# Optimization experiments

Measured on AMD Instinct MI355X. Metric: run time of the kernel, lower is better.

## Reference

```python
import jax, jax.numpy as jnp
import numpy as np

B = 8
S = 512  # seq_len


def setup_inputs() -> dict:
    key = jax.random.key(0)
    kx, kw, kb = jax.random.split(key, 3)
    x = jax.random.normal(kx, (B, S, S), dtype=jnp.float32)
    # Padded block of per-diagonal Linear weights: W[i, k, j] is weight[k, j]
    # of nn.Linear(i+1, i+1); entries with k > i or j > i are zero.
    i_d = jnp.arange(S)[:, None, None]
    k_d = jnp.arange(S)[None, :, None]
    j_d = jnp.arange(S)[None, None, :]
    wmask = ((k_d <= i_d) & (j_d <= i_d)).astype(jnp.float32)
    W = jax.random.normal(kw, (S, S, S), dtype=jnp.float32) * 0.02 * wmask
    bmask = (jnp.arange(S)[None, :] <= jnp.arange(S)[:, None]).astype(jnp.float32)
    b = jax.random.normal(kb, (S, S), dtype=jnp.float32) * 0.02 * bmask
    return {"x": x, "W": W, "b": b}


def reference(x, W, b):
    # For each anti-diagonal i (positions (r, i-r), r=0..i, with r+c=i<S):
    #   gather d = x[:, r, i-r], apply Linear_i: out = d @ W_i^T + b_i,
    #   scatter back reversed: x[:, r, i-r] = out[i-r]  =>  x[b,r,c]=out[b,r+c,c].
    S_ = x.shape[-1]
    i_idx = jnp.arange(S_)[:, None]   # diagonal index
    r_idx = jnp.arange(S_)[None, :]   # position along diagonal
    cols = (i_idx - r_idx) % S_
    valid = (r_idx <= i_idx)[None]                       # [1,S,S]
    # D[b, i, r] = x[b, r, i-r] for r<=i else 0
    D = jnp.where(valid, x[:, r_idx, cols], 0.0)         # [B,S,S]
    # Batched per-diagonal matmul: out[b,i,k] = sum_j W[i,k,j] D[b,i,j] + b[i,k]
    out = jnp.einsum('bij,ikj->bik', D, W) + b[None]     # [B,S,S]
    # Scatter back with reversal: x[b,r,c] = out[b, r+c, c] when r+c < S
    rr = jnp.arange(S_)[:, None]
    cc = jnp.arange(S_)[None, :]
    diag = rr + cc
    ok = (diag < S_)[None]
    new_x = jnp.where(ok, out[:, jnp.minimum(diag, S_ - 1), cc], x)
    return new_x
```

## Files before the change

kernel.cpp:

```cpp
#include <hip/hip_runtime.h>

#define S 512
#define NB 8
#define KT 128
#define JT 32

__global__ __launch_bounds__(256) void tail_copy_kernel(const float* __restrict__ x,
                                                        float* __restrict__ out) {
  int idx = blockIdx.x * 256 + threadIdx.x;
  int c = idx & (S - 1);
  int r = (idx >> 9) & (S - 1);
  if (r + c >= S) out[idx] = x[idx];
}

__global__ __launch_bounds__(256, 4) void diag_linear_kernel(const float* __restrict__ x,
                                                             const float* __restrict__ W,
                                                             const float* __restrict__ bias,
                                                             float* __restrict__ out) {
  __shared__ __align__(16) float WtBuf[JT * KT];
  __shared__ __align__(16) float DlBuf[S * NB];

  const int i  = (S - 1) - (int)blockIdx.x;
  const int k0 = (int)blockIdx.y * KT;
  if (k0 > i) return;

  const int tid  = threadIdx.x;
  const int wave = tid >> 6;
  const int lane = tid & 63;

  const int jend = (i + JT) & ~(JT - 1);
  const int T    = jend >> 5;

  for (int idx = tid; idx < jend * NB; idx += 256) {
    const int j = idx >> 3;
    const int b = idx & 7;
    DlBuf[idx] = (j <= i) ? x[b * (S * S) + j * S + (i - j)] : 0.0f;
  }

  const int kl_r = tid & (KT - 1);
  const int h    = tid >> 7;
  const int  k_r     = k0 + kl_r;
  const bool krow_ok = (k_r <= i);
  const float* wrow  = W + ((size_t)i * S + k_r) * S + (h << 4);

  float acc[2][NB];
#pragma unroll
  for (int m = 0; m < 2; ++m)
#pragma unroll
    for (int b = 0; b < NB; ++b) acc[m][b] = 0.0f;

  float4 v[2][4];
  if (!krow_ok) {
#pragma unroll
    for (int g = 0; g < 2; ++g)
#pragma unroll
      for (int q = 0; q < 4; ++q) v[g][q] = make_float4(0.f, 0.f, 0.f, 0.f);
  }

#define LOAD_GRP(g, J0)                                                        \
  if (krow_ok) {                                                               \
    _Pragma("unroll")                                                          \
    for (int q = 0; q < 4; ++q)                                                \
      v[g][q] = *(const float4*)(wrow + (J0) + 4 * q);                         \
  }

  LOAD_GRP(0, 0)
  if (T > 1) LOAD_GRP(1, 32)

  for (int t = 0; t < T; ++t) {
    const int pb = t & 1;
    const int j0 = t << 5;
    __syncthreads();
    {
      const float4* vv = v[pb];
#pragma unroll
      for (int q = 0; q < 4; ++q) {
        const int jl = (h << 4) + (q << 2);
        WtBuf[(jl + 0) * KT + kl_r] = vv[q].x;
        WtBuf[(jl + 1) * KT + kl_r] = vv[q].y;
        WtBuf[(jl + 2) * KT + kl_r] = vv[q].z;
        WtBuf[(jl + 3) * KT + kl_r] = vv[q].w;
      }
    }
    const int tn = t + 2;
    if (tn < T) LOAD_GRP(pb, tn << 5)
    __syncthreads();

#pragma unroll
    for (int uu = 0; uu < 8; ++uu) {
      const int jl = (wave << 3) + uu;
      const float2 wv = *(const float2*)&WtBuf[jl * KT + (lane << 1)];
      const float4 dA = *(const float4*)&DlBuf[(j0 + jl) * NB];
      const float4 dB = *(const float4*)&DlBuf[(j0 + jl) * NB + 4];
      const float wm[2] = {wv.x, wv.y};
#pragma unroll
      for (int m = 0; m < 2; ++m) {
        acc[m][0] = fmaf(wm[m], dA.x, acc[m][0]);
        acc[m][1] = fmaf(wm[m], dA.y, acc[m][1]);
        acc[m][2] = fmaf(wm[m], dA.z, acc[m][2]);
        acc[m][3] = fmaf(wm[m], dA.w, acc[m][3]);
        acc[m][4] = fmaf(wm[m], dB.x, acc[m][4]);
        acc[m][5] = fmaf(wm[m], dB.y, acc[m][5]);
        acc[m][6] = fmaf(wm[m], dB.z, acc[m][6]);
        acc[m][7] = fmaf(wm[m], dB.w, acc[m][7]);
      }
    }
  }

  __syncthreads();
  float* Racc = WtBuf;

  for (int w = 0; w < 4; ++w) {
    if (wave == w) {
#pragma unroll
      for (int b = 0; b < NB; ++b) {
        float2* p = (float2*)&Racc[b * KT + (lane << 1)];
        float2 cur = make_float2(acc[0][b], acc[1][b]);
        if (w != 0) {
          float2 old = *p;
          cur.x += old.x; cur.y += old.y;
        }
        *p = cur;
      }
    }
    __syncthreads();
  }

  {
    const int k = k0 + kl_r;
    if (k <= i) {
      const float bv = bias[i * S + k];
      const int r = i - k;
#pragma unroll
      for (int bq = 0; bq < 4; ++bq) {
        const int b = (h << 2) + bq;
        out[b * (S * S) + r * S + k] = Racc[b * KT + kl_r] + bv;
      }
    }
  }
}

extern "C" void kernel_launch(void* const* d_in, const int* in_sizes, int n_in,
                              void* d_out, int out_size, void* d_ws, size_t ws_size,
                              hipStream_t stream) {
  const float* x    = (const float*)d_in[0];
  const float* W    = (const float*)d_in[1];
  const float* bias = (const float*)d_in[2];
  float* out = (float*)d_out;

  (void)d_ws; (void)ws_size; (void)in_sizes; (void)n_in; (void)out_size;

  tail_copy_kernel<<<dim3((NB * S * S) / 256), 256, 0, stream>>>(x, out);
  diag_linear_kernel<<<dim3(S, S / KT), 256, 0, stream>>>(x, W, bias, out);
}
```

Baseline: 701.5 us.

## Keep W rows in registers per thread and reduce partial sums with shuffles

Each thread now owns half of one W row. It accumulates directly from the W values it loaded into registers, so the shared-memory transpose of W and the two block barriers per j-tile are gone. The final cross-thread reduction uses a pair-wise __shfl_xor instead of a four-step shared-memory accumulation with barriers. Launch bounds are raised to allow more resident blocks, and rows beyond the diagonal now exit early. The trade-off is a longer serial FMA chain per thread, with less parallelism across waves per row.

Measured after the change: 1.207 ms. 72.0% more time.

```diff
diff --git a/kernel.cpp b/kernel.cpp
--- a/kernel.cpp
+++ b/kernel.cpp
@@ -13,11 +13,10 @@
   if (r + c >= S) out[idx] = x[idx];
 }
 
-__global__ __launch_bounds__(256, 4) void diag_linear_kernel(const float* __restrict__ x,
+__global__ __launch_bounds__(256, 6) void diag_linear_kernel(const float* __restrict__ x,
                                                              const float* __restrict__ W,
                                                              const float* __restrict__ bias,
                                                              float* __restrict__ out) {
-  __shared__ __align__(16) float WtBuf[JT * KT];
   __shared__ __align__(16) float DlBuf[S * NB];
 
   const int i  = (S - 1) - (int)blockIdx.x;
@@ -25,9 +24,6 @@
   if (k0 > i) return;
 
   const int tid  = threadIdx.x;
-  const int wave = tid >> 6;
-  const int lane = tid & 63;
-
   const int jend = (i + JT) & ~(JT - 1);
   const int T    = jend >> 5;
 
@@ -36,107 +32,67 @@
     const int b = idx & 7;
     DlBuf[idx] = (j <= i) ? x[b * (S * S) + j * S + (i - j)] : 0.0f;
   }
+  __syncthreads();
 
-  const int kl_r = tid & (KT - 1);
-  const int h    = tid >> 7;
-  const int  k_r     = k0 + kl_r;
-  const bool krow_ok = (k_r <= i);
-  const float* wrow  = W + ((size_t)i * S + k_r) * S + (h << 4);
+  const int kl = tid >> 1;
+  const int h  = tid & 1;
+  const int k  = k0 + kl;
+  if (k > i) return;
 
-  float acc[2][NB];
+  const float* wrow = W + ((size_t)i * S + k) * S + (h << 4);
+
+  float acc[NB];
 #pragma unroll
-  for (int m = 0; m < 2; ++m)
-#pragma unroll
-    for (int b = 0; b < NB; ++b) acc[m][b] = 0.0f;
+  for (int b = 0; b < NB; ++b) acc[b] = 0.0f;
 
   float4 v[2][4];
-  if (!krow_ok) {
-#pragma unroll
-    for (int g = 0; g < 2; ++g)
-#pragma unroll
-      for (int q = 0; q < 4; ++q) v[g][q] = make_float4(0.f, 0.f, 0.f, 0.f);
-  }
-
-#define LOAD_GRP(g, J0)                                                        \
-  if (krow_ok) {                                                               \
-    _Pragma("unroll")                                                          \
-    for (int q = 0; q < 4; ++q)                                                \
-      v[g][q] = *(const float4*)(wrow + (J0) + 4 * q);                         \
+#define LOAD_GRP(g, t)                                                         \
+  {                                                                            \
+    const float* p = wrow + ((t) << 5);                                        \
+    v[g][0] = *(const float4*)(p);                                             \
+    v[g][1] = *(const float4*)(p + 4);                                         \
+    v[g][2] = *(const float4*)(p + 8);                                         \
+    v[g][3] = *(const float4*)(p + 12);                                        \
   }
 
   LOAD_GRP(0, 0)
-  if (T > 1) LOAD_GRP(1, 32)
+  if (T > 1) LOAD_GRP(1, 1)
 
   for (int t = 0; t < T; ++t) {
-    const int pb = t & 1;
-    const int j0 = t << 5;
-    __syncthreads();
-    {
-      const float4* vv = v[pb];
+    const int g  = t & 1;
+    const int j0 = (t << 5) + (h << 4);
 #pragma unroll
-      for (int q = 0; q < 4; ++q) {
-        const int jl = (h << 4) + (q << 2);
-        WtBuf[(jl + 0) * KT + kl_r] = vv[q].x;
-        WtBuf[(jl + 1) * KT + kl_r] = vv[q].y;
-        WtBuf[(jl + 2) * KT + kl_r] = vv[q].z;
-        WtBuf[(jl + 3) * KT + kl_r] = vv[q].w;
+    for (int q = 0; q < 4; ++q) {
+      const float wq[4] = {v[g][q].x, v[g][q].y, v[g][q].z, v[g][q].w};
+#pragma unroll
+      for (int e = 0; e < 4; ++e) {
+        const int j = j0 + (q << 2) + e;
+        const float4 dA = *(const float4*)&DlBuf[j * NB];
+        const float4 dB = *(const float4*)&DlBuf[j * NB + 4];
+        const float w = wq[e];
+        acc[0] = fmaf(w, dA.x, acc[0]);
+        acc[1] = fmaf(w, dA.y, acc[1]);
+        acc[2] = fmaf(w, dA.z, acc[2]);
+        acc[3] = fmaf(w, dA.w, acc[3]);
+        acc[4] = fmaf(w, dB.x, acc[4]);
+        acc[5] = fmaf(w, dB.y, acc[5]);
+        acc[6] = fmaf(w, dB.z, acc[6]);
+        acc[7] = fmaf(w, dB.w, acc[7]);
       }
     }
     const int tn = t + 2;
-    if (tn < T) LOAD_GRP(pb, tn << 5)
-    __syncthreads();
+    if (tn < T) LOAD_GRP(g, tn)
+  }
 
 #pragma unroll
-    for (int uu = 0; uu < 8; ++uu) {
-      const int jl = (wave << 3) + uu;
-      const float2 wv = *(const float2*)&WtBuf[jl * KT + (lane << 1)];
-      const float4 dA = *(const float4*)&DlBuf[(j0 + jl) * NB];
-      const float4 dB = *(const float4*)&DlBuf[(j0 + jl) * NB + 4];
-      const float wm[2] = {wv.x, wv.y};
+  for (int b = 0; b < NB; ++b) acc[b] += __shfl_xor(acc[b], 1);
+
+  const float bv = bias[i * S + k];
+  const int r = i - k;
 #pragma unroll
-      for (int m = 0; m < 2; ++m) {
-        acc[m][0] = fmaf(wm[m], dA.x, acc[m][0]);
-        acc[m][1] = fmaf(wm[m], dA.y, acc[m][1]);
-        acc[m][2] = fmaf(wm[m], dA.z, acc[m][2]);
-        acc[m][3] = fmaf(wm[m], dA.w, acc[m][3]);
-        acc[m][4] = fmaf(wm[m], dB.x, acc[m][4]);
-        acc[m][5] = fmaf(wm[m], dB.y, acc[m][5]);
-        acc[m][6] = fmaf(wm[m], dB.z, acc[m][6]);
-        acc[m][7] = fmaf(wm[m], dB.w, acc[m][7]);
-      }
-    }
-  }
-
-  __syncthreads();
-  float* Racc = WtBuf;
-
-  for (int w = 0; w < 4; ++w) {
-    if (wave == w) {
-#pragma unroll
-      for (int b = 0; b < NB; ++b) {
-        float2* p = (float2*)&Racc[b * KT + (lane << 1)];
-        float2 cur = make_float2(acc[0][b], acc[1][b]);
-        if (w != 0) {
-          float2 old = *p;
-          cur.x += old.x; cur.y += old.y;
-        }
-        *p = cur;
-      }
-    }
-    __syncthreads();
-  }
-
-  {
-    const int k = k0 + kl_r;
-    if (k <= i) {
-      const float bv = bias[i * S + k];
-      const int r = i - k;
-#pragma unroll
-      for (int bq = 0; bq < 4; ++bq) {
-        const int b = (h << 2) + bq;
-        out[b * (S * S) + r * S + k] = Racc[b * KT + kl_r] + bv;
-      }
-    }
+  for (int bq = 0; bq < 4; ++bq) {
+    const int b = (h << 2) + bq;
+    out[b * (S * S) + r * S + k] = acc[b] + bv;
   }
 }
 
```
